# Optimization experiments

Hardware: AMD Instinct MI355X
Metric: run time of the kernel (lower is better)

Reference implementation:

```python
import jax, jax.numpy as jnp
import numpy as np

B, S, D_IN = 32, 128, 17
D_PT, D_PAIR, D_OUT = 64, 128, 64
EPS = 1e-5


def _gelu(x):
    return jax.nn.gelu(x, approximate=False)  # torch nn.GELU default (erf)


def _bn(h, g, b):
    # BatchNorm1d (training mode): stats over batch and pair dims, per channel
    mean = h.mean(axis=(0, 1))
    var = h.var(axis=(0, 1))  # biased, matching torch normalization
    return (h - mean) * jax.lax.rsqrt(var + EPS) * g + b


def setup_inputs() -> dict:
    key = jax.random.key(0)
    ks = jax.random.split(key, 8)
    s = lambda k, shp, fan: jax.random.normal(k, shp, jnp.float32) * (1.0 / np.sqrt(fan))
    return {
        "x": jax.random.normal(ks[0], (B, S, D_IN), jnp.float32),
        # pointwise MLP: 17 -> 64 -> 64
        "w1": s(ks[1], (D_IN, D_PT), D_IN), "b1": jnp.zeros((D_PT,), jnp.float32),
        "w2": s(ks[2], (D_PT, D_PT), D_PT), "b2": jnp.zeros((D_PT,), jnp.float32),
        # pair MLP: 128 -> 128 -> 128 (input = 2 * D_PT)
        "wp1": s(ks[3], (2 * D_PT, D_PAIR), 2 * D_PT), "bp1": jnp.zeros((D_PAIR,), jnp.float32),
        "wp2": s(ks[4], (D_PAIR, D_PAIR), D_PAIR), "bp2": jnp.zeros((D_PAIR,), jnp.float32),
        # embed: BN(128) -> Conv1d(128,64,1) -> BN(64) -> GELU -> Conv1d(64,64,1) -> BN(64)
        "g0": jnp.ones((D_PAIR,), jnp.float32), "be0": jnp.zeros((D_PAIR,), jnp.float32),
        "wc1": s(ks[5], (D_PAIR, D_OUT), D_PAIR), "bc1": jnp.zeros((D_OUT,), jnp.float32),
        "g1": jnp.ones((D_OUT,), jnp.float32), "be1": jnp.zeros((D_OUT,), jnp.float32),
        "wc2": s(ks[6], (D_OUT, D_OUT), D_OUT), "bc2": jnp.zeros((D_OUT,), jnp.float32),
        "g2": jnp.ones((D_OUT,), jnp.float32), "be2": jnp.zeros((D_OUT,), jnp.float32),
    }


def reference(x, w1, b1, w2, b2, wp1, bp1, wp2, bp2,
              g0, be0, wc1, bc1, g1, be1, wc2, bc2, g2, be2):
    seq_len = x.shape[1]
    # pointwise MLP
    h = _gelu(x @ w1 + b1)
    h = _gelu(h @ w2 + b2)  # [B, S, D_PT]
    # tril pair gather (xi = features of particle j, xj = of particle i,
    # matching x_rep[b, a, c] = x[b, c] semantics in the torch code)
    i_idx, j_idx = jnp.tril_indices(seq_len)
    xi = h[:, j_idx, :]  # [B, P, D_PT]
    xj = h[:, i_idx, :]
    xij = jnp.concatenate([xi, xj], axis=-1)  # [B, P, 2*D_PT]
    # pair MLP
    e = _gelu(xij @ wp1 + bp1)
    e = _gelu(e @ wp2 + bp2)  # [B, P, D_PAIR]
    # embed stack (Conv1d k=1 == channel-wise linear)
    e = _bn(e, g0, be0)
    e = _gelu(_bn(e @ wc1 + bc1, g1, be1))
    e = _bn(e @ wc2 + bc2, g2, be2)  # [B, P, D_OUT]
    # symmetric scatter into dense pairwise output
    y = jnp.zeros((x.shape[0], seq_len, seq_len, e.shape[-1]), e.dtype)
    y = y.at[:, i_idx, j_idx, :].set(e)
    y = y.at[:, j_idx, i_idx, :].set(e)
    return y
```

## Files before the change

kernel.cpp:

```cpp
#include <hip/hip_runtime.h>
#include <hip/hip_bf16.h>
#include <math.h>

#define BB 32
#define SS 128
#define DIN 17
#define DPT 64
#define DPA 128
#define DOU 64
#define NP 8256
#define NROWS (BB * NP)
#define NCHUNK (NROWS / 128)
#define EPSF 1e-5f

typedef __hip_bfloat16 bf16;
typedef __attribute__((ext_vector_type(8))) short short8;
typedef __attribute__((ext_vector_type(16))) float f32x16;
typedef __attribute__((ext_vector_type(4))) float f32x4;
typedef __attribute__((ext_vector_type(4))) int int4v;
typedef __attribute__((ext_vector_type(4))) unsigned int uint4v;

#define MFMA32(a, b, c) __builtin_amdgcn_mfma_f32_32x32x16_bf16(a, b, c, 0, 0, 0)

__device__ __forceinline__ float bf2f(short u) {
    return __builtin_bit_cast(float, ((unsigned int)(unsigned short)u) << 16);
}

__device__ __forceinline__ void plswap(unsigned int& a, unsigned int& b) {
    asm("v_permlane32_swap_b32 %0, %1" : "+v"(a), "+v"(b));
}
__device__ __forceinline__ unsigned int cvtpk(float lo, float hi) {
    unsigned int r;
    asm("v_cvt_pk_bf16_f32 %0, %1, %2" : "=v"(r) : "v"(lo), "v"(hi));
    return r;
}

__device__ __forceinline__ void xform(const f32x16& a, short8& o0, short8& o1) {
    unsigned int w[8];
#pragma unroll
    for (int j = 0; j < 8; ++j) w[j] = cvtpk(a[2 * j], a[2 * j + 1]);
    plswap(w[0], w[2]);
    plswap(w[1], w[3]);
    plswap(w[4], w[6]);
    plswap(w[5], w[7]);
    uint4v u0 = {w[0], w[1], w[2], w[3]};
    uint4v u1 = {w[4], w[5], w[6], w[7]};
    o0 = __builtin_bit_cast(short8, u0);
    o1 = __builtin_bit_cast(short8, u1);
}

__device__ __forceinline__ float gelu_exact(float x) {
    float z = fabsf(x) * 0.7071067811865476f;
    float t = __builtin_amdgcn_rcpf(fmaf(0.3275911f, z, 1.0f));
    float p = fmaf(t, 1.061405429f, -1.453152027f);
    p = fmaf(t, p, 1.421413741f);
    p = fmaf(t, p, -0.284496736f);
    p = fmaf(t, p, 0.254829592f);
    p *= t;
    float e = __expf(-z * z);
    float erfz = 1.0f - p * e;
    float s = copysignf(erfz, x);
    return 0.5f * x * (1.0f + s);
}

__global__ void k_pairs(int* __restrict__ pairIJ) {
    int p = blockIdx.x * blockDim.x + threadIdx.x;
    if (p >= NP) return;
    int i = (int)((sqrtf(8.0f * (float)p + 1.0f) - 1.0f) * 0.5f);
    while ((i * (i + 1)) / 2 > p) --i;
    while (((i + 1) * (i + 2)) / 2 <= p) ++i;
    int j = p - (i * (i + 1)) / 2;
    pairIJ[p] = (i << 8) | j;
}

__global__ void k_pack(const float* __restrict__ wp1, const float* __restrict__ wp2,
                       const float* __restrict__ wc2, bf16* __restrict__ fragP1,
                       bf16* __restrict__ fragP2, bf16* __restrict__ fragC2) {
    int id = blockIdx.x * 256 + threadIdx.x;
    if (id < 16384) {
        int f = id >> 9, lane = (id >> 3) & 63, i = id & 7;
        int mt = f >> 3, s = f & 7;
        int k = s * 16 + (lane >> 5) * 8 + i;
        int m = mt * 32 + (lane & 31);
        fragP1[id] = __float2bfloat16(wp1[k * DPA + m]);
    } else if (id < 32768) {
        int rem = id - 16384;
        int f = rem >> 9, lane = (rem >> 3) & 63, i = rem & 7;
        int mt = f >> 3, s = f & 7;
        int k = s * 16 + (lane >> 5) * 8 + i;
        int m = mt * 32 + (lane & 31);
        fragP2[rem] = __float2bfloat16(wp2[k * DPA + m]);
    } else if (id < 36864) {
        int rem = id - 32768;
        int f = rem >> 9, lane = (rem >> 3) & 63, i = rem & 7;
        int mt = f >> 2, s = f & 3;
        int k = s * 16 + (lane >> 5) * 8 + i;
        int m = mt * 32 + (lane & 31);
        fragC2[rem] = __float2bfloat16(wc2[k * DOU + m]);
    }
}

__global__ void k_fold(const float* __restrict__ a0, const float* __restrict__ d0,
                       const float* __restrict__ wc1, const float* __restrict__ bc1,
                       bf16* __restrict__ fragC1, float* __restrict__ bc1p) {
    int id = blockIdx.x * 256 + threadIdx.x;
    if (id < 8192) {
        int f = id >> 9, lane = (id >> 3) & 63, i = id & 7;
        int mt = f >> 3, s = f & 7;
        int k = s * 16 + (lane >> 5) * 8 + i;
        int m = mt * 32 + (lane & 31);
        fragC1[id] = __float2bfloat16(a0[k] * wc1[k * DOU + m]);
    } else if (id < 8192 + 64) {
        int c = id - 8192;
        float s = bc1[c];
        for (int k = 0; k < DPA; ++k) s = fmaf(d0[k], wc1[k * DOU + c], s);
        bc1p[c] = s;
    }
}

__global__ void k_h(const float* __restrict__ x, const float* __restrict__ w1,
                    const float* __restrict__ b1, const float* __restrict__ w2,
                    const float* __restrict__ b2, bf16* __restrict__ h) {
    __shared__ float h1[4][DPT];
    int t = threadIdx.x;
    int rs = t >> 6;
    int c = t & 63;
    int r = blockIdx.x * 4 + rs;
    const float* xr = x + (size_t)r * DIN;
    float acc = b1[c];
#pragma unroll
    for (int k = 0; k < DIN; ++k) acc += xr[k] * w1[k * DPT + c];
    h1[rs][c] = gelu_exact(acc);
    __syncthreads();
    float acc2 = b2[c];
#pragma unroll
    for (int k = 0; k < DPT; ++k) acc2 += h1[rs][k] * w2[k * DPT + c];
    h[(size_t)r * DPT + c] = __float2bfloat16(gelu_exact(acc2));
}

__global__ __launch_bounds__(256) void k_e0m(
    const bf16* __restrict__ h, const int* __restrict__ pairIJ,
    const short8* __restrict__ fragP1, const short8* __restrict__ fragP2,
    const float* __restrict__ bp1, const float* __restrict__ bp2,
    bf16* __restrict__ e0, float* __restrict__ part) {
    __shared__ __align__(16) char buf[32768];
    int t = threadIdx.x;
    int w = t >> 6, l = t & 63;
    int l31 = l & 31, lhi = l >> 5;
    int row0 = blockIdx.x * 128;
    int prow = w * 32 + l31;

#pragma unroll
    for (int q = 0; q < 8; ++q) {
        int task = t + 256 * q;
        int rr = task >> 4, slot = task & 15;
        int n = row0 + rr;
        int b = n / NP, p = n - b * NP;
        int ij = pairIJ[p];
        int src = (slot < 8) ? (ij & 255) : (ij >> 8);
        int4v v = *(const int4v*)(h + (((size_t)(b * SS + src)) << 6) + ((slot & 7) << 3));
        *(int4v*)(buf + rr * 256 + ((slot * 16) ^ ((rr & 15) << 4))) = v;
    }
    __syncthreads();

    f32x16 acc[4];
#pragma unroll
    for (int mt = 0; mt < 4; ++mt)
#pragma unroll
        for (int g = 0; g < 4; ++g) {
            f32x4 bv = *(const f32x4*)(bp1 + mt * 32 + g * 8 + lhi * 4);
#pragma unroll
            for (int j = 0; j < 4; ++j) acc[mt][g * 4 + j] = bv[j];
        }
#pragma unroll
    for (int s = 0; s < 8; ++s) {
        short8 bx = *(const short8*)(buf + prow * 256 +
                                     (((s * 2 + lhi) * 16) ^ ((prow & 15) << 4)));
        acc[0] = MFMA32(fragP1[(0 * 8 + s) * 64 + l], bx, acc[0]);
        acc[1] = MFMA32(fragP1[(1 * 8 + s) * 64 + l], bx, acc[1]);
        acc[2] = MFMA32(fragP1[(2 * 8 + s) * 64 + l], bx, acc[2]);
        acc[3] = MFMA32(fragP1[(3 * 8 + s) * 64 + l], bx, acc[3]);
    }

    short8 B2[8];
#pragma unroll
    for (int mt = 0; mt < 4; ++mt) {
#pragma unroll
        for (int r = 0; r < 16; ++r) acc[mt][r] = gelu_exact(acc[mt][r]);
        xform(acc[mt], B2[2 * mt], B2[2 * mt + 1]);
    }

    f32x16 acc2[4];
#pragma unroll
    for (int mt = 0; mt < 4; ++mt)
#pragma unroll
        for (int g = 0; g < 4; ++g) {
            f32x4 bv = *(const f32x4*)(bp2 + mt * 32 + g * 8 + lhi * 4);
#pragma unroll
            for (int j = 0; j < 4; ++j) acc2[mt][g * 4 + j] = bv[j];
        }
#pragma unroll
    for (int s = 0; s < 8; ++s) {
        acc2[0] = MFMA32(fragP2[(0 * 8 + s) * 64 + l], B2[s], acc2[0]);
        acc2[1] = MFMA32(fragP2[(1 * 8 + s) * 64 + l], B2[s], acc2[1]);
        acc2[2] = MFMA32(fragP2[(2 * 8 + s) * 64 + l], B2[s], acc2[2]);
        acc2[3] = MFMA32(fragP2[(3 * 8 + s) * 64 + l], B2[s], acc2[3]);
    }
    __syncthreads();

#pragma unroll
    for (int mt = 0; mt < 4; ++mt) {
#pragma unroll
        for (int r = 0; r < 16; ++r) acc2[mt][r] = gelu_exact(acc2[mt][r]);
        short8 o0, o1;
        xform(acc2[mt], o0, o1);
        int slot0 = 4 * mt + lhi, slot1 = 4 * mt + 2 + lhi;
        *(short8*)(buf + prow * 256 + ((slot0 * 16) ^ ((prow & 15) << 4))) = o0;
        *(short8*)(buf + prow * 256 + ((slot1 * 16) ^ ((prow & 15) << 4))) = o1;
    }
    __syncthreads();

    float sum[8], sq[8];
#pragma unroll
    for (int i = 0; i < 8; ++i) { sum[i] = 0.f; sq[i] = 0.f; }
    int slot = t & 15;
#pragma unroll
    for (int q = 0; q < 8; ++q) {
        int rr = (t >> 4) + 16 * q;
        short8 v = *(const short8*)(buf + rr * 256 + ((slot * 16) ^ ((rr & 15) << 4)));
        *(short8*)(e0 + (size_t)(row0 + rr) * DPA + slot * 8) = v;
#pragma unroll
        for (int i = 0; i < 8; ++i) {
            float f = bf2f(v[i]);
            sum[i] += f;
            sq[i] += f * f;
        }
    }
    __syncthreads();
    float* bb = (float*)buf;
#pragma unroll
    for (int i = 0; i < 8; ++i) {
        bb[t * 16 + i] = sum[i];
        bb[t * 16 + 8 + i] = sq[i];
    }
    __syncthreads();
    {
        int c = t & 127, isq = t >> 7;
        float s = 0.f;
#pragma unroll
        for (int g = 0; g < 16; ++g)
            s += bb[((c >> 3) + 16 * g) * 16 + isq * 8 + (c & 7)];
        part[(size_t)blockIdx.x * 256 + t] = s;
    }
}

__global__ void k_stats(const float* __restrict__ part, int nch, int nblk,
                        float* __restrict__ a, float* __restrict__ d,
                        const float* __restrict__ g, const float* __restrict__ be) {
    int c = blockIdx.x;
    __shared__ float ssum[256], ssq[256];
    float s = 0.f, q = 0.f;
    for (int bidx = threadIdx.x; bidx < nblk; bidx += 256) {
        s += part[(size_t)bidx * (2 * nch) + c];
        q += part[(size_t)bidx * (2 * nch) + nch + c];
    }
    ssum[threadIdx.x] = s;
    ssq[threadIdx.x] = q;
    __syncthreads();
    for (int w = 128; w > 0; w >>= 1) {
        if ((int)threadIdx.x < w) {
            ssum[threadIdx.x] += ssum[threadIdx.x + w];
            ssq[threadIdx.x] += ssq[threadIdx.x + w];
        }
        __syncthreads();
    }
    if (threadIdx.x == 0) {
        float mean = ssum[0] / (float)NROWS;
        float var = ssq[0] / (float)NROWS - mean * mean;
        float rstd = rsqrtf(var + EPSF);
        float aa = g[c] * rstd;
        a[c] = aa;
        d[c] = be[c] - mean * aa;
    }
}

__global__ __launch_bounds__(256) void k_e1m(
    const bf16* __restrict__ e0, const short8* __restrict__ fragC1,
    const float* __restrict__ bc1p, bf16* __restrict__ e1,
    float* __restrict__ part) {
    __shared__ __align__(16) char buf[16384];
    int t = threadIdx.x;
    int w = t >> 6, l = t & 63;
    int l31 = l & 31, lhi = l >> 5;
    int row0 = blockIdx.x * 128;
    int prow = w * 32 + l31;

    short8 B[8];
#pragma unroll
    for (int s = 0; s < 8; ++s)
        B[s] = *(const short8*)(e0 + (size_t)(row0 + prow) * DPA + s * 16 + lhi * 8);

    f32x16 acc[2];
#pragma unroll
    for (int mt = 0; mt < 2; ++mt)
#pragma unroll
        for (int g = 0; g < 4; ++g) {
            f32x4 bv = *(const f32x4*)(bc1p + mt * 32 + g * 8 + lhi * 4);
#pragma unroll
            for (int j = 0; j < 4; ++j) acc[mt][g * 4 + j] = bv[j];
        }
#pragma unroll
    for (int s = 0; s < 8; ++s) {
        acc[0] = MFMA32(fragC1[(0 * 8 + s) * 64 + l], B[s], acc[0]);
        acc[1] = MFMA32(fragC1[(1 * 8 + s) * 64 + l], B[s], acc[1]);
    }

#pragma unroll
    for (int mt = 0; mt < 2; ++mt) {
        short8 o0, o1;
        xform(acc[mt], o0, o1);
        int slot0 = 4 * mt + lhi, slot1 = 4 * mt + 2 + lhi;
        *(short8*)(buf + prow * 128 + ((slot0 * 16) ^ ((prow & 7) << 4))) = o0;
        *(short8*)(buf + prow * 128 + ((slot1 * 16) ^ ((prow & 7) << 4))) = o1;
    }
    __syncthreads();

    float sum[8], sq[8];
#pragma unroll
    for (int i = 0; i < 8; ++i) { sum[i] = 0.f; sq[i] = 0.f; }
    int slot = t & 7;
#pragma unroll
    for (int q = 0; q < 4; ++q) {
        int rr = (t >> 3) + 32 * q;
        short8 v = *(const short8*)(buf + rr * 128 + ((slot * 16) ^ ((rr & 7) << 4)));
        *(short8*)(e1 + (size_t)(row0 + rr) * DOU + slot * 8) = v;
#pragma unroll
        for (int i = 0; i < 8; ++i) {
            float f = bf2f(v[i]);
            sum[i] += f;
            sq[i] += f * f;
        }
    }
    __syncthreads();
    float* bb = (float*)buf;
#pragma unroll
    for (int i = 0; i < 8; ++i) {
        bb[t * 16 + i] = sum[i];
        bb[t * 16 + 8 + i] = sq[i];
    }
    __syncthreads();
    if (t < 128) {
        int c = t & 63, isq = t >> 6;
        float s = 0.f;
#pragma unroll
        for (int g = 0; g < 32; ++g)
            s += bb[((c >> 3) + 8 * g) * 16 + isq * 8 + (c & 7)];
        part[(size_t)blockIdx.x * 128 + t] = s;
    }
}

__global__ __launch_bounds__(256) void k_e2m(
    const bf16* __restrict__ e1, const float* __restrict__ a1,
    const float* __restrict__ d1, const short8* __restrict__ fragC2,
    const float* __restrict__ bc2, bf16* __restrict__ e2,
    float* __restrict__ part) {
    __shared__ __align__(16) char buf[16384];
    int t = threadIdx.x;
    int w = t >> 6, l = t & 63;
    int l31 = l & 31, lhi = l >> 5;
    int row0 = blockIdx.x * 128;
    int prow = w * 32 + l31;

    short8 B[4];
#pragma unroll
    for (int s = 0; s < 4; ++s) {
        short8 raw = *(const short8*)(e1 + (size_t)(row0 + prow) * DOU + s * 16 + lhi * 8);
        int c0 = s * 16 + lhi * 8;
        f32x4 av0 = *(const f32x4*)(a1 + c0), av1 = *(const f32x4*)(a1 + c0 + 4);
        f32x4 dv0 = *(const f32x4*)(d1 + c0), dv1 = *(const f32x4*)(d1 + c0 + 4);
        float gg[8];
#pragma unroll
        for (int i = 0; i < 4; ++i) gg[i] = gelu_exact(fmaf(bf2f(raw[i]), av0[i], dv0[i]));
#pragma unroll
        for (int i = 0; i < 4; ++i) gg[4 + i] = gelu_exact(fmaf(bf2f(raw[4 + i]), av1[i], dv1[i]));
        uint4v u = {cvtpk(gg[0], gg[1]), cvtpk(gg[2], gg[3]),
                    cvtpk(gg[4], gg[5]), cvtpk(gg[6], gg[7])};
        B[s] = __builtin_bit_cast(short8, u);
    }

    f32x16 acc[2];
#pragma unroll
    for (int mt = 0; mt < 2; ++mt)
#pragma unroll
        for (int g = 0; g < 4; ++g) {
            f32x4 bv = *(const f32x4*)(bc2 + mt * 32 + g * 8 + lhi * 4);
#pragma unroll
            for (int j = 0; j < 4; ++j) acc[mt][g * 4 + j] = bv[j];
        }
#pragma unroll
    for (int s = 0; s < 4; ++s) {
        acc[0] = MFMA32(fragC2[(0 * 4 + s) * 64 + l], B[s], acc[0]);
        acc[1] = MFMA32(fragC2[(1 * 4 + s) * 64 + l], B[s], acc[1]);
    }

#pragma unroll
    for (int mt = 0; mt < 2; ++mt) {
        short8 o0, o1;
        xform(acc[mt], o0, o1);
        int slot0 = 4 * mt + lhi, slot1 = 4 * mt + 2 + lhi;
        *(short8*)(buf + prow * 128 + ((slot0 * 16) ^ ((prow & 7) << 4))) = o0;
        *(short8*)(buf + prow * 128 + ((slot1 * 16) ^ ((prow & 7) << 4))) = o1;
    }
    __syncthreads();

    float sum[8], sq[8];
#pragma unroll
    for (int i = 0; i < 8; ++i) { sum[i] = 0.f; sq[i] = 0.f; }
    int slot = t & 7;
#pragma unroll
    for (int q = 0; q < 4; ++q) {
        int rr = (t >> 3) + 32 * q;
        short8 v = *(const short8*)(buf + rr * 128 + ((slot * 16) ^ ((rr & 7) << 4)));
        *(short8*)(e2 + (size_t)(row0 + rr) * DOU + slot * 8) = v;
#pragma unroll
        for (int i = 0; i < 8; ++i) {
            float f = bf2f(v[i]);
            sum[i] += f;
            sq[i] += f * f;
        }
    }
    __syncthreads();
    float* bb = (float*)buf;
#pragma unroll
    for (int i = 0; i < 8; ++i) {
        bb[t * 16 + i] = sum[i];
        bb[t * 16 + 8 + i] = sq[i];
    }
    __syncthreads();
    if (t < 128) {
        int c = t & 63, isq = t >> 6;
        float s = 0.f;
#pragma unroll
        for (int g = 0; g < 32; ++g)
            s += bb[((c >> 3) + 8 * g) * 16 + isq * 8 + (c & 7)];
        part[(size_t)blockIdx.x * 128 + t] = s;
    }
}

__global__ void k_out(const bf16* __restrict__ e2, const int* __restrict__ pairIJ,
                      const float* __restrict__ a2, const float* __restrict__ d2,
                      float* __restrict__ y) {
    int t = threadIdx.x;
    int n = blockIdx.x * 32 + (t >> 3);
    int c0 = (t & 7) * 8;
    int b = n / NP, p = n - b * NP;
    int ij = pairIJ[p];
    int ii = ij >> 8, jj = ij & 255;
    short8 raw = *(const short8*)(e2 + (size_t)n * DOU + c0);
    f32x4 aLo = *(const f32x4*)(a2 + c0), aHi = *(const f32x4*)(a2 + c0 + 4);
    f32x4 dLo = *(const f32x4*)(d2 + c0), dHi = *(const f32x4*)(d2 + c0 + 4);
    f32x4 v0, v1;
#pragma unroll
    for (int i = 0; i < 4; ++i) v0[i] = fmaf(bf2f(raw[i]), aLo[i], dLo[i]);
#pragma unroll
    for (int i = 0; i < 4; ++i) v1[i] = fmaf(bf2f(raw[4 + i]), aHi[i], dHi[i]);
    float* y1 = y + ((size_t)(b * SS + ii) * SS + jj) * DOU + c0;
    float* y2 = y + ((size_t)(b * SS + jj) * SS + ii) * DOU + c0;
    *(f32x4*)y1 = v0;
    *(f32x4*)(y1 + 4) = v1;
    *(f32x4*)y2 = v0;
    *(f32x4*)(y2 + 4) = v1;
}

extern "C" void kernel_launch(void* const* d_in, const int* in_sizes, int n_in,
                              void* d_out, int out_size, void* d_ws, size_t ws_size,
                              hipStream_t stream) {
    const float* x   = (const float*)d_in[0];
    const float* w1  = (const float*)d_in[1];
    const float* b1  = (const float*)d_in[2];
    const float* w2  = (const float*)d_in[3];
    const float* b2  = (const float*)d_in[4];
    const float* wp1 = (const float*)d_in[5];
    const float* bp1 = (const float*)d_in[6];
    const float* wp2 = (const float*)d_in[7];
    const float* bp2 = (const float*)d_in[8];
    const float* g0  = (const float*)d_in[9];
    const float* be0 = (const float*)d_in[10];
    const float* wc1 = (const float*)d_in[11];
    const float* bc1 = (const float*)d_in[12];
    const float* g1  = (const float*)d_in[13];
    const float* be1 = (const float*)d_in[14];
    const float* wc2 = (const float*)d_in[15];
    const float* bc2 = (const float*)d_in[16];
    const float* g2  = (const float*)d_in[17];
    const float* be2 = (const float*)d_in[18];

    char* ws = (char*)d_ws;
    const size_t OFF_PAIR   = 0;
    const size_t OFF_H      = 33280;
    const size_t OFF_PART   = 557568;
    const size_t OFF_FRAGP1 = 2671104;
    const size_t OFF_FRAGP2 = 2703872;
    const size_t OFF_FRAGC1 = 2736640;
    const size_t OFF_FRAGC2 = 2753024;
    const size_t OFF_BC1P   = 2761216;
    const size_t OFF_A0 = 2761472, OFF_D0 = 2761984;
    const size_t OFF_A1 = 2762496, OFF_D1 = 2762752;
    const size_t OFF_A2 = 2763008, OFF_D2 = 2763264;
    const size_t OFF_E2 = 2763520;

    int*   pairIJ = (int*)(ws + OFF_PAIR);
    bf16*  h      = (bf16*)(ws + OFF_H);
    float* part   = (float*)(ws + OFF_PART);
    bf16*  fragP1 = (bf16*)(ws + OFF_FRAGP1);
    bf16*  fragP2 = (bf16*)(ws + OFF_FRAGP2);
    bf16*  fragC1 = (bf16*)(ws + OFF_FRAGC1);
    bf16*  fragC2 = (bf16*)(ws + OFF_FRAGC2);
    float* bc1p   = (float*)(ws + OFF_BC1P);
    float* a0 = (float*)(ws + OFF_A0);
    float* d0 = (float*)(ws + OFF_D0);
    float* a1 = (float*)(ws + OFF_A1);
    float* d1 = (float*)(ws + OFF_D1);
    float* a2 = (float*)(ws + OFF_A2);
    float* d2 = (float*)(ws + OFF_D2);
    bf16*  e2 = (bf16*)(ws + OFF_E2);

    bf16* e0 = (bf16*)d_out;
    bf16* e1 = (bf16*)((char*)d_out + (size_t)NROWS * DPA * sizeof(bf16));
    float* y = (float*)d_out;

    k_pairs<<<(NP + 255) / 256, 256, 0, stream>>>(pairIJ);
    k_pack<<<144, 256, 0, stream>>>(wp1, wp2, wc2, fragP1, fragP2, fragC2);
    k_h<<<(BB * SS) / 4, 256, 0, stream>>>(x, w1, b1, w2, b2, h);
    k_e0m<<<NCHUNK, 256, 0, stream>>>(h, pairIJ, (const short8*)fragP1,
                                      (const short8*)fragP2, bp1, bp2, e0, part);
    k_stats<<<DPA, 256, 0, stream>>>(part, DPA, NCHUNK, a0, d0, g0, be0);
    k_fold<<<33, 256, 0, stream>>>(a0, d0, wc1, bc1, fragC1, bc1p);
    k_e1m<<<NCHUNK, 256, 0, stream>>>(e0, (const short8*)fragC1, bc1p, e1, part);
    k_stats<<<DOU, 256, 0, stream>>>(part, DOU, NCHUNK, a1, d1, g1, be1);
    k_e2m<<<NCHUNK, 256, 0, stream>>>(e1, a1, d1, (const short8*)fragC2, bc2, e2, part);
    k_stats<<<DOU, 256, 0, stream>>>(part, DOU, NCHUNK, a2, d2, g2, be2);
    k_out<<<NROWS / 32, 256, 0, stream>>>(e2, pairIJ, a2, d2, y);
}
```

Before: 192.7 us.

## Stage pair-MLP weights in LDS/registers, gather inputs directly, use tanh GELU

In the pair-MLP kernel, half of the first-layer weight fragments are now held in registers. The other half and all second-layer fragments are copied once per block into a 48KB LDS buffer, replacing repeated global fragment loads inside the MFMA loops. Each lane gathers its own pair-row inputs straight into registers instead of going through an LDS staging pass. The GELU helper switches from an erf polynomial to the tanh-form approximation written via exp and reciprocal, which is cheaper but numerically different from the exact-erf reference. The conv kernels also preload their weight fragments into registers, and the pair kernel asks for two blocks per CU, which adds register and LDS pressure.

```diff
diff --git a/kernel.cpp b/kernel.cpp
--- a/kernel.cpp
+++ b/kernel.cpp
@@ -50,17 +50,11 @@
 }
 
 __device__ __forceinline__ float gelu_exact(float x) {
-    float z = fabsf(x) * 0.7071067811865476f;
-    float t = __builtin_amdgcn_rcpf(fmaf(0.3275911f, z, 1.0f));
-    float p = fmaf(t, 1.061405429f, -1.453152027f);
-    p = fmaf(t, p, 1.421413741f);
-    p = fmaf(t, p, -0.284496736f);
-    p = fmaf(t, p, 0.254829592f);
-    p *= t;
-    float e = __expf(-z * z);
-    float erfz = 1.0f - p * e;
-    float s = copysignf(erfz, x);
-    return 0.5f * x * (1.0f + s);
+    float x2 = x * x;
+    float m = fmaf(0.0356774081f, x2, 0.7978845608f);
+    float e = __expf(2.0f * x * m);
+    float r = __builtin_amdgcn_rcpf(e + 1.0f);
+    return fmaf(-x, r, x);
 }
 
 __global__ void k_pairs(int* __restrict__ pairIJ) {
@@ -138,28 +132,37 @@
     h[(size_t)r * DPT + c] = __float2bfloat16(gelu_exact(acc2));
 }
 
-__global__ __launch_bounds__(256) void k_e0m(
+__global__ __launch_bounds__(256, 2) void k_e0m(
     const bf16* __restrict__ h, const int* __restrict__ pairIJ,
     const short8* __restrict__ fragP1, const short8* __restrict__ fragP2,
     const float* __restrict__ bp1, const float* __restrict__ bp2,
     bf16* __restrict__ e0, float* __restrict__ part) {
-    __shared__ __align__(16) char buf[32768];
+    __shared__ __align__(16) char lds[49152];
     int t = threadIdx.x;
     int w = t >> 6, l = t & 63;
     int l31 = l & 31, lhi = l >> 5;
     int row0 = blockIdx.x * 128;
     int prow = w * 32 + l31;
 
-#pragma unroll
-    for (int q = 0; q < 8; ++q) {
-        int task = t + 256 * q;
-        int rr = task >> 4, slot = task & 15;
-        int n = row0 + rr;
-        int b = n / NP, p = n - b * NP;
-        int ij = pairIJ[p];
-        int src = (slot < 8) ? (ij & 255) : (ij >> 8);
-        int4v v = *(const int4v*)(h + (((size_t)(b * SS + src)) << 6) + ((slot & 7) << 3));
-        *(int4v*)(buf + rr * 256 + ((slot * 16) ^ ((rr & 15) << 4))) = v;
+    for (int u = t; u < 3072; u += 256) {
+        short8 v = (u < 1024) ? fragP1[1024 + u] : fragP2[u - 1024];
+        *(short8*)(lds + u * 16) = v;
+    }
+
+    short8 Wa[16];
+#pragma unroll
+    for (int i = 0; i < 16; ++i) Wa[i] = fragP1[i * 64 + l];
+
+    int n = row0 + prow;
+    int b = n / NP, p = n - b * NP;
+    int ij = pairIJ[p];
+    const bf16* hj = h + (((size_t)(b * SS + (ij & 255))) << 6);
+    const bf16* hi = h + (((size_t)(b * SS + (ij >> 8))) << 6);
+    short8 bx[8];
+#pragma unroll
+    for (int s = 0; s < 4; ++s) {
+        bx[s] = *(const short8*)(hj + s * 16 + lhi * 8);
+        bx[s + 4] = *(const short8*)(hi + s * 16 + lhi * 8);
     }
     __syncthreads();
 
@@ -174,12 +177,12 @@
         }
 #pragma unroll
     for (int s = 0; s < 8; ++s) {
-        short8 bx = *(const short8*)(buf + prow * 256 +
-                                     (((s * 2 + lhi) * 16) ^ ((prow & 15) << 4)));
-        acc[0] = MFMA32(fragP1[(0 * 8 + s) * 64 + l], bx, acc[0]);
-        acc[1] = MFMA32(fragP1[(1 * 8 + s) * 64 + l], bx, acc[1]);
-        acc[2] = MFMA32(fragP1[(2 * 8 + s) * 64 + l], bx, acc[2]);
-        acc[3] = MFMA32(fragP1[(3 * 8 + s) * 64 + l], bx, acc[3]);
+        short8 a2 = *(const short8*)(lds + (s * 64 + l) * 16);
+        short8 a3 = *(const short8*)(lds + ((8 + s) * 64 + l) * 16);
+        acc[0] = MFMA32(Wa[s], bx[s], acc[0]);
+        acc[1] = MFMA32(Wa[8 + s], bx[s], acc[1]);
+        acc[2] = MFMA32(a2, bx[s], acc[2]);
+        acc[3] = MFMA32(a3, bx[s], acc[3]);
     }
 
     short8 B2[8];
@@ -201,22 +204,28 @@
         }
 #pragma unroll
     for (int s = 0; s < 8; ++s) {
-        acc2[0] = MFMA32(fragP2[(0 * 8 + s) * 64 + l], B2[s], acc2[0]);
-        acc2[1] = MFMA32(fragP2[(1 * 8 + s) * 64 + l], B2[s], acc2[1]);
-        acc2[2] = MFMA32(fragP2[(2 * 8 + s) * 64 + l], B2[s], acc2[2]);
-        acc2[3] = MFMA32(fragP2[(3 * 8 + s) * 64 + l], B2[s], acc2[3]);
-    }
-    __syncthreads();
-
+#pragma unroll
+        for (int mt = 0; mt < 4; ++mt) {
+            short8 a = *(const short8*)(lds + 16384 + ((mt * 8 + s) * 64 + l) * 16);
+            acc2[mt] = MFMA32(a, B2[s], acc2[mt]);
+        }
+    }
+
+    short8 o[4][2];
 #pragma unroll
     for (int mt = 0; mt < 4; ++mt) {
 #pragma unroll
         for (int r = 0; r < 16; ++r) acc2[mt][r] = gelu_exact(acc2[mt][r]);
-        short8 o0, o1;
-        xform(acc2[mt], o0, o1);
+        xform(acc2[mt], o[mt][0], o[mt][1]);
+    }
+    __syncthreads();
+
+    char* stage = lds + 16384;
+#pragma unroll
+    for (int mt = 0; mt < 4; ++mt) {
         int slot0 = 4 * mt + lhi, slot1 = 4 * mt + 2 + lhi;
-        *(short8*)(buf + prow * 256 + ((slot0 * 16) ^ ((prow & 15) << 4))) = o0;
-        *(short8*)(buf + prow * 256 + ((slot1 * 16) ^ ((prow & 15) << 4))) = o1;
+        *(short8*)(stage + prow * 256 + ((slot0 * 16) ^ ((prow & 15) << 4))) = o[mt][0];
+        *(short8*)(stage + prow * 256 + ((slot1 * 16) ^ ((prow & 15) << 4))) = o[mt][1];
     }
     __syncthreads();
 
@@ -227,7 +236,7 @@
 #pragma unroll
     for (int q = 0; q < 8; ++q) {
         int rr = (t >> 4) + 16 * q;
-        short8 v = *(const short8*)(buf + rr * 256 + ((slot * 16) ^ ((rr & 15) << 4)));
+        short8 v = *(const short8*)(stage + rr * 256 + ((slot * 16) ^ ((rr & 15) << 4)));
         *(short8*)(e0 + (size_t)(row0 + rr) * DPA + slot * 8) = v;
 #pragma unroll
         for (int i = 0; i < 8; ++i) {
@@ -237,7 +246,7 @@
         }
     }
     __syncthreads();
-    float* bb = (float*)buf;
+    float* bb = (float*)stage;
 #pragma unroll
     for (int i = 0; i < 8; ++i) {
         bb[t * 16 + i] = sum[i];
@@ -295,6 +304,9 @@
     int row0 = blockIdx.x * 128;
     int prow = w * 32 + l31;
 
+    short8 Wc[16];
+#pragma unroll
+    for (int i = 0; i < 16; ++i) Wc[i] = fragC1[i * 64 + l];
     short8 B[8];
 #pragma unroll
     for (int s = 0; s < 8; ++s)
@@ -311,8 +323,8 @@
         }
 #pragma unroll
     for (int s = 0; s < 8; ++s) {
-        acc[0] = MFMA32(fragC1[(0 * 8 + s) * 64 + l], B[s], acc[0]);
-        acc[1] = MFMA32(fragC1[(1 * 8 + s) * 64 + l], B[s], acc[1]);
+        acc[0] = MFMA32(Wc[s], B[s], acc[0]);
+        acc[1] = MFMA32(Wc[8 + s], B[s], acc[1]);
     }
 
 #pragma unroll
@@ -371,6 +383,10 @@
     int row0 = blockIdx.x * 128;
     int prow = w * 32 + l31;
 
+    short8 Wc[8];
+#pragma unroll
+    for (int s = 0; s < 8; ++s) Wc[s] = fragC2[s * 64 + l];
+
     short8 B[4];
 #pragma unroll
     for (int s = 0; s < 4; ++s) {
@@ -399,8 +415,8 @@
         }
 #pragma unroll
     for (int s = 0; s < 4; ++s) {
-        acc[0] = MFMA32(fragC2[(0 * 4 + s) * 64 + l], B[s], acc[0]);
-        acc[1] = MFMA32(fragC2[(1 * 4 + s) * 64 + l], B[s], acc[1]);
+        acc[0] = MFMA32(Wc[s], B[s], acc[0]);
+        acc[1] = MFMA32(Wc[4 + s], B[s], acc[1]);
     }
 
 #pragma unroll
```

After: 158.1 us. 1.22x faster.
